# Kernel tuning notes

Measured on AMD Instinct MI355X. Metric: run time of the kernel, lower is better.

## Reference

```python
import jax, jax.numpy as jnp
import numpy as np
from jax import lax

EPS = 1e-5


def setup_inputs() -> dict:
    key = jax.random.key(0)
    ks = jax.random.split(key, 8)
    b, c_in, h, w = 16, 256, 64, 64
    c_out, kh, n_exp = 512, 3, 8
    fan_in = c_in * kh * kh
    bound_w = float(np.sqrt(6.0 / fan_in))  # kaiming_uniform a=sqrt(5) -> U(-sqrt(6/fan_in), +)
    bound_b = float(1.0 / np.sqrt(fan_in))
    return {
        "x": jax.random.normal(ks[0], (b, c_in, h, w), dtype=jnp.float32),
        "expert_weight": jax.random.uniform(ks[1], (n_exp, c_out, c_in, kh, kh), jnp.float32, -bound_w, bound_w),
        "expert_bias": jax.random.uniform(ks[2], (n_exp, c_out), jnp.float32, -bound_b, bound_b),
        "fc_w": jax.random.uniform(ks[3], (n_exp, c_in), jnp.float32, -1.0 / np.sqrt(c_in), 1.0 / np.sqrt(c_in)),
        "fc_b": jax.random.uniform(ks[4], (n_exp,), jnp.float32, -1.0 / np.sqrt(c_in), 1.0 / np.sqrt(c_in)),
        "bn_gamma": jnp.ones((c_out,), jnp.float32),
        "bn_beta": jnp.zeros((c_out,), jnp.float32),
    }


def reference(x, expert_weight, expert_bias, fc_w, fc_b, bn_gamma, bn_beta):
    # --- route_func: GAP -> Linear -> sigmoid -> (b, k) ---
    pooled = x.mean(axis=(2, 3))                       # (b, c_in)
    routing = jax.nn.sigmoid(pooled @ fc_w.T + fc_b)   # (b, k)

    # --- per-sample combined kernels and biases ---
    comb_w = jnp.einsum('bk,koihw->boihw', routing, expert_weight)  # (b, c_out, c_in, kh, kw)
    comb_b = routing @ expert_bias                                  # (b, c_out)

    # --- per-sample conv (equivalent of groups=b grouped conv) ---
    def conv_one(xi, wi):
        # xi: (c_in, h, w), wi: (c_out, c_in, kh, kw)
        return lax.conv_general_dilated(
            xi[None], wi, window_strides=(1, 1), padding=[(1, 1), (1, 1)],
            rhs_dilation=(1, 1), dimension_numbers=('NCHW', 'OIHW', 'NCHW'))[0]

    out = jax.vmap(conv_one)(x, comb_w) + comb_b[:, :, None, None]  # (b, c_out, h, w)

    # --- BatchNorm2d (training mode: batch statistics) ---
    mean = out.mean(axis=(0, 2, 3))
    var = out.var(axis=(0, 2, 3))
    out = (out - mean[None, :, None, None]) * (bn_gamma * lax.rsqrt(var + EPS))[None, :, None, None] \
          + bn_beta[None, :, None, None]

    # --- LeakyReLU(0.1) ---
    return jnp.where(out > 0, out, 0.1 * out)
```

## Files before the change

### kernel.cpp

```cpp
#include <hip/hip_runtime.h>
#include <hip/hip_bf16.h>
#include <stdint.h>

typedef unsigned short u16;
typedef short bf16x8 __attribute__((ext_vector_type(8)));
typedef float f32x4 __attribute__((ext_vector_type(4)));
typedef u16 u16x8 __attribute__((ext_vector_type(8)));

#define DEVFN static __device__ __forceinline__

#define NB 16
#define CIN 256
#define HH 64
#define WW 64
#define COUT 512
#define NPX 4096
#define NSTEP 72

DEVFN u16 bf16_rne(float f){
  union { float f; uint32_t u; } v; v.f = f;
  uint32_t u = v.u;
  return (u16)((u + 0x7fffu + ((u >> 16) & 1u)) >> 16);
}

DEVFN void gload16(const void* g, void* l){
  __builtin_amdgcn_global_load_lds((const __attribute__((address_space(1))) void*)g,
                                   (__attribute__((address_space(3))) void*)l,
                                   16, 0, 0);
}

#define VMWAIT(N) asm volatile("s_waitcnt vmcnt(" #N ")" ::: "memory")
#define BARRIER() do { __builtin_amdgcn_s_barrier(); \
                       __builtin_amdgcn_sched_barrier(0); \
                       asm volatile("" ::: "memory"); } while(0)

__global__ void k_route(const float* __restrict__ pooled, const float* __restrict__ fcw,
                        const float* __restrict__ fcb, float* __restrict__ routing){
  int bk = blockIdx.x;
  int b = bk >> 3, k = bk & 7;
  int l = threadIdx.x;
  float4 pv = ((const float4*)(pooled + b*CIN))[l];
  float4 wv = ((const float4*)(fcw   + k*CIN))[l];
  float s = pv.x*wv.x + pv.y*wv.y + pv.z*wv.z + pv.w*wv.w;
  for (int o = 32; o; o >>= 1) s += __shfl_down(s, o);
  if (l == 0) routing[b*8 + k] = 1.0f / (1.0f + __expf(-(s * (1.0f/(float)NPX) + fcb[k])));
}

__global__ void k_cbias(const float* __restrict__ routing, const float* __restrict__ eb,
                        float* __restrict__ cbias){
  int idx = blockIdx.x*256 + threadIdx.x;
  int b = idx >> 9, co = idx & 511;
  float s = 0.f;
  for (int k = 0; k < 8; k++) s += routing[b*8+k] * eb[k*COUT + co];
  cbias[idx] = s;
}

__global__ void k_wcomb(const float* __restrict__ routing, const float* __restrict__ ew,
                        u16* __restrict__ wc){
  int blk  = blockIdx.x;
  int step = blk >> 6;
  int cog  = blk & 63;
  int cb = step / 9, rs = step - cb*9;
  int t = threadIdx.x;
  int ci = t & 31, co = cog*8 + (t >> 5);
  int cig = cb*32 + ci;
  float wv[8];
#pragma unroll
  for (int k = 0; k < 8; k++)
    wv[k] = ew[(size_t)((k*COUT + co)*CIN + cig)*9 + rs];
  for (int b = 0; b < NB; b++){
    float s = 0.f;
#pragma unroll
    for (int k = 0; k < 8; k++) s += routing[b*8+k] * wv[k];
    wc[((size_t)(b*NSTEP + step)*COUT + co)*32 + ci] = bf16_rne(s);
  }
}

__global__ void k_halo(u16* __restrict__ xt){
  int blk = blockIdx.x;
  int b = blk / 66, row = blk - b*66;
  uint32_t* base = (uint32_t*)(xt + ((size_t)(b*66 + row))*68*256);
  int t = threadIdx.x;
  if (row == 0 || row == 65){
    for (int i = t; i < 8704; i += 256) base[i] = 0;
  } else {
    for (int i = t; i < 512; i += 256){
      int idx = (i < 128) ? i : (8320 + (i - 128));
      base[idx] = 0;
    }
  }
}

__global__ void k_xprep(const float* __restrict__ x, u16* __restrict__ xt,
                        float* __restrict__ pooled){
  int blk = blockIdx.x;
  int ctile = blk & 3;
  int h = (blk >> 2) & 63;
  int b = blk >> 8;
  __shared__ u16 S[64][66];
  int t = threadIdx.x;
  {
    int ci_l = t >> 2, w0 = (t & 3) * 16;
    const float4* src = (const float4*)(x + ((size_t)((b*CIN + ctile*64 + ci_l)*HH + h)*WW + w0));
    float4 a = src[0], bb = src[1], c = src[2], d = src[3];
    u16* row = &S[ci_l][w0];
    row[0]=bf16_rne(a.x);  row[1]=bf16_rne(a.y);  row[2]=bf16_rne(a.z);  row[3]=bf16_rne(a.w);
    row[4]=bf16_rne(bb.x); row[5]=bf16_rne(bb.y); row[6]=bf16_rne(bb.z); row[7]=bf16_rne(bb.w);
    row[8]=bf16_rne(c.x);  row[9]=bf16_rne(c.y);  row[10]=bf16_rne(c.z); row[11]=bf16_rne(c.w);
    row[12]=bf16_rne(d.x); row[13]=bf16_rne(d.y); row[14]=bf16_rne(d.z); row[15]=bf16_rne(d.w);
    float s = a.x+a.y+a.z+a.w + bb.x+bb.y+bb.z+bb.w + c.x+c.y+c.z+c.w + d.x+d.y+d.z+d.w;
    s += __shfl_down(s, 2);
    s += __shfl_down(s, 1);
    if ((t & 3) == 0) atomicAdd(&pooled[b*CIN + ctile*64 + ci_l], s);
  }
  __syncthreads();
  {
    int w_l = t >> 2, cig = (t & 3) * 16;
    u16x8 v0, v1;
#pragma unroll
    for (int j = 0; j < 8; j++){ v0[j] = S[cig+j][w_l]; v1[j] = S[cig+8+j][w_l]; }
    u16* dst = xt + ((size_t)(b*66 + h + 1)*68 + (w_l + 1))*CIN + ctile*64 + cig;
    *(u16x8*)(dst)     = v0;
    *(u16x8*)(dst + 8) = v1;
  }
}

#define XBYTES 17408
#define WBYTES 8192

DEVFN void stage_w(const u16* __restrict__ wstep, char* dst, int wv, int l){
#pragma unroll
  for (int i = 0; i < 2; i++){
    int q = i*256 + wv*64 + l;
    int co_l = q >> 2, j = q & 3;
    gload16(wstep + co_l*32 + ((j ^ ((co_l >> 1) & 3)) << 3), dst + (i*256 + wv*64)*16);
  }
  __builtin_amdgcn_sched_barrier(0);
}

DEVFN void stage_x(const u16* __restrict__ xtb, int h0, int cioff, char* dst, int wv, int l){
#pragma unroll
  for (int i = 0; i < 5; i++){
    int qb = i*256 + wv*64;
    if (qb >= 1088) qb -= 1088;
    int q = qb + l;
    int t2 = q >> 2;
    int lr = (t2 * 964) >> 16;
    int c  = t2 - lr*68;
    int j  = q & 3;
    gload16(xtb + ((size_t)(h0 + lr)*68 + c)*CIN + cioff + ((j ^ ((c >> 1) & 3)) << 3),
            dst + qb*16);
  }
  __builtin_amdgcn_sched_barrier(0);
}

template<int RS>
DEVFN void conv_step(int cb, char* ldsbase, char* Xb,
                     const u16* __restrict__ wcb,
                     int wv, int l, int wn, int l15, int kbq, int byteA0,
                     f32x4 acc[4][4])
{
  constexpr int r = RS / 3, s = RS - r*3;
  const char* Wc = ldsbase + (RS % 3)*WBYTES;
  char* Wp       = ldsbase + ((RS + 2) % 3)*WBYTES;

  int c0 = l15 + s;
  int byteB0 = ((wn + r)*68 + c0)*64 + ((kbq ^ ((c0 >> 1) & 3)) << 4);
  bf16x8 af[4], bfr[4];
#pragma unroll
  for (int m = 0; m < 4; m++) af[m]  = *(const bf16x8*)(Wc + byteA0 + m*1024);
#pragma unroll
  for (int n = 0; n < 4; n++) bfr[n] = *(const bf16x8*)(Xb + byteB0 + n*1024);

  if constexpr (RS <= 6) {
    stage_w(wcb + (size_t)(cb*9 + RS + 2)*(COUT*32), Wp, wv, l);
  } else {
    if (cb != 7) stage_w(wcb + (size_t)(cb*9 + RS + 2)*(COUT*32), Wp, wv, l);
  }

  if constexpr (RS == 7) {
    if (cb == 7) { VMWAIT(0); } else { VMWAIT(2); }
  } else {
    VMWAIT(2);
  }
  BARRIER();

  __builtin_amdgcn_s_setprio(1);
#pragma unroll
  for (int m = 0; m < 4; m++)
#pragma unroll
    for (int n = 0; n < 4; n++)
      acc[m][n] = __builtin_amdgcn_mfma_f32_16x16x32_bf16(af[m], bfr[n], acc[m][n], 0, 0, 0);
  __builtin_amdgcn_s_setprio(0);
}

DEVFN void conv_step8(int cb, char* ldsbase, char* Xb,
                      const u16* __restrict__ xtb, const u16* __restrict__ wcb, int h0,
                      int wv, int l, int wn, int l15, int kbq, int byteA0,
                      f32x4 acc[4][4])
{
  const char* Wc = ldsbase + 2*WBYTES;
  char* Wp       = ldsbase + 1*WBYTES;
  int c0 = l15 + 2;
  int byteB0 = ((wn + 2)*68 + c0)*64 + ((kbq ^ ((c0 >> 1) & 3)) << 4);
  bf16x8 af[4], bfr[4];
#pragma unroll
  for (int m = 0; m < 4; m++) af[m]  = *(const bf16x8*)(Wc + byteA0 + m*1024);
#pragma unroll
  for (int n = 0; n < 4; n++) bfr[n] = *(const bf16x8*)(Xb + byteB0 + n*1024);

  BARRIER();

  stage_w(wcb + (size_t)(cb*9 + 10)*(COUT*32), Wp, wv, l);
  stage_x(xtb, h0, (cb+1)*32, Xb, wv, l);

  __builtin_amdgcn_s_setprio(1);
#pragma unroll
  for (int m = 0; m < 4; m++)
#pragma unroll
    for (int n = 0; n < 4; n++)
      acc[m][n] = __builtin_amdgcn_mfma_f32_16x16x32_bf16(af[m], bfr[n], acc[m][n], 0, 0, 0);
  __builtin_amdgcn_s_setprio(0);

  VMWAIT(0);
  BARRIER();
}

DEVFN void conv_step8_last(char* ldsbase, char* Xb,
                           int wn, int l15, int kbq, int byteA0,
                           f32x4 acc[4][4])
{
  const char* Wc = ldsbase + 2*WBYTES;
  int c0 = l15 + 2;
  int byteB0 = ((wn + 2)*68 + c0)*64 + ((kbq ^ ((c0 >> 1) & 3)) << 4);
  bf16x8 af[4], bfr[4];
#pragma unroll
  for (int m = 0; m < 4; m++) af[m]  = *(const bf16x8*)(Wc + byteA0 + m*1024);
#pragma unroll
  for (int n = 0; n < 4; n++) bfr[n] = *(const bf16x8*)(Xb + byteB0 + n*1024);
#pragma unroll
  for (int m = 0; m < 4; m++)
#pragma unroll
    for (int n = 0; n < 4; n++)
      acc[m][n] = __builtin_amdgcn_mfma_f32_16x16x32_bf16(af[m], bfr[n], acc[m][n], 0, 0, 0);
}

__global__ __launch_bounds__(256, 3) void k_conv(
    const u16* __restrict__ xt, const u16* __restrict__ wc,
    const float* __restrict__ cbias, float* __restrict__ out, u16* __restrict__ obf,
    float* __restrict__ ssum, float* __restrict__ ssq)
{
  __shared__ char lds[3*WBYTES + XBYTES];
  char* Xb = lds + 3*WBYTES;

  int hw = blockIdx.x;
  int lb = (hw & 7) * 256 + (hw >> 3);
  int b  = lb >> 7;
  int ct = (lb >> 5) & 3;
  int pt = lb & 31;
  int h0 = pt * 2;

  int t = threadIdx.x, l = t & 63, wv = t >> 6;
  int wm = wv >> 1, wn = wv & 1;
  int l15 = l & 15, kbq = l >> 4;

  const u16* xtb = xt + (size_t)b * 66*68*CIN;
  const u16* wcb = wc + (size_t)(b*NSTEP) * COUT*32 + ct*128*32;

  f32x4 acc[4][4];
#pragma unroll
  for (int m = 0; m < 4; m++)
#pragma unroll
    for (int n = 0; n < 4; n++) acc[m][n] = (f32x4){0.f,0.f,0.f,0.f};

  const int byteA0 = (wm*64 + l15)*64 + ((kbq ^ ((l15 >> 1) & 3)) << 4);

  stage_x(xtb, h0, 0, Xb, wv, l);
  stage_w(wcb,           lds + 0*WBYTES, wv, l);
  stage_w(wcb + COUT*32, lds + 1*WBYTES, wv, l);
  VMWAIT(2);
  BARRIER();

  for (int cb = 0; cb < 8; cb++){
    conv_step<0>(cb, lds, Xb, wcb, wv,l,wn,l15,kbq,byteA0, acc);
    conv_step<1>(cb, lds, Xb, wcb, wv,l,wn,l15,kbq,byteA0, acc);
    conv_step<2>(cb, lds, Xb, wcb, wv,l,wn,l15,kbq,byteA0, acc);
    conv_step<3>(cb, lds, Xb, wcb, wv,l,wn,l15,kbq,byteA0, acc);
    conv_step<4>(cb, lds, Xb, wcb, wv,l,wn,l15,kbq,byteA0, acc);
    conv_step<5>(cb, lds, Xb, wcb, wv,l,wn,l15,kbq,byteA0, acc);
    conv_step<6>(cb, lds, Xb, wcb, wv,l,wn,l15,kbq,byteA0, acc);
    conv_step<7>(cb, lds, Xb, wcb, wv,l,wn,l15,kbq,byteA0, acc);
    if (cb < 7) conv_step8(cb, lds, Xb, xtb, wcb, h0, wv,l,wn,l15,kbq,byteA0, acc);
    else        conv_step8_last(lds, Xb, wn,l15,kbq,byteA0, acc);
  }

  int co_t = ct*128 + wm*64 + (kbq << 2);
  int px_t = pt*128 + wn*64 + l15;
#pragma unroll
  for (int m = 0; m < 4; m++){
#pragma unroll
    for (int rg = 0; rg < 4; rg++){
      int co = co_t + m*16 + rg;
      float bias = cbias[b*COUT + co];
      float s1 = 0.f, s2 = 0.f;
      size_t base = ((size_t)b * COUT + co) * NPX + px_t;
#pragma unroll
      for (int n = 0; n < 4; n++){
        float v = acc[m][n][rg] + bias;
        if (obf) obf[base + n*16] = bf16_rne(v);
        else     out[base + n*16] = v;
        s1 += v; s2 += v*v;
      }
#pragma unroll
      for (int o = 8; o; o >>= 1){ s1 += __shfl_xor(s1, o); s2 += __shfl_xor(s2, o); }
      if (l15 == 0){ atomicAdd(&ssum[co], s1); atomicAdd(&ssq[co], s2); }
    }
  }
}

__global__ void k_stats(const float* __restrict__ ssum, const float* __restrict__ ssq,
                        const float* __restrict__ gamma, const float* __restrict__ beta,
                        float* __restrict__ sc, float* __restrict__ sh){
  int co = blockIdx.x*256 + threadIdx.x;
  const float invN = 1.0f / 65536.0f;
  float m  = ssum[co] * invN;
  float var = ssq[co] * invN - m*m;
  float scale = gamma[co] * rsqrtf(var + 1e-5f);
  sc[co] = scale;
  sh[co] = beta[co] - m*scale;
}

__global__ void k_norm(float* __restrict__ out, const float* __restrict__ sc,
                       const float* __restrict__ sh){
  const int NF4 = (NB*COUT*NPX)/4;
  int idx = blockIdx.x*256 + threadIdx.x;
  float4* o4 = (float4*)out;
  for (int i = idx; i < NF4; i += 2048*256){
    float4 v = o4[i];
    int co = (i >> 10) & 511;
    float a = sc[co], d = sh[co];
    v.x = fmaf(v.x, a, d); v.y = fmaf(v.y, a, d);
    v.z = fmaf(v.z, a, d); v.w = fmaf(v.w, a, d);
    v.x = v.x > 0.f ? v.x : 0.1f*v.x;
    v.y = v.y > 0.f ? v.y : 0.1f*v.y;
    v.z = v.z > 0.f ? v.z : 0.1f*v.z;
    v.w = v.w > 0.f ? v.w : 0.1f*v.w;
    o4[i] = v;
  }
}

__global__ void k_norm_bf16(const u16* __restrict__ obf, float* __restrict__ out,
                            const float* __restrict__ sc, const float* __restrict__ sh){
  const int NG = (NB*COUT*NPX)/8;
  int idx = blockIdx.x*256 + threadIdx.x;
  for (int g = idx; g < NG; g += 2048*256){
    u16x8 v = *(const u16x8*)(obf + (size_t)g*8);
    int co = (g >> 9) & 511;
    float a = sc[co], d = sh[co];
    float vv[8];
#pragma unroll
    for (int j = 0; j < 8; j++){
      union{ uint32_t u; float f; } c; c.u = ((uint32_t)(u16)v[j]) << 16;
      float w = fmaf(c.f, a, d);
      vv[j] = w > 0.f ? w : 0.1f*w;
    }
    float4* o4 = (float4*)(out + (size_t)g*8);
    o4[0] = (float4){vv[0],vv[1],vv[2],vv[3]};
    o4[1] = (float4){vv[4],vv[5],vv[6],vv[7]};
  }
}

extern "C" void kernel_launch(void* const* d_in, const int* in_sizes, int n_in,
                              void* d_out, int out_size, void* d_ws, size_t ws_size,
                              hipStream_t stream) {
  const float* x     = (const float*)d_in[0];
  const float* ew    = (const float*)d_in[1];
  const float* eb    = (const float*)d_in[2];
  const float* fcw   = (const float*)d_in[3];
  const float* fcb   = (const float*)d_in[4];
  const float* gamma = (const float*)d_in[5];
  const float* beta  = (const float*)d_in[6];
  float* out = (float*)d_out;

  char* ws = (char*)d_ws;
  const size_t XT_BYTES  = (size_t)NB*66*68*CIN*2;
  const size_t WC_BYTES  = (size_t)NB*NSTEP*COUT*32*2;
  const size_t FL_BYTES  = 65536;
  const size_t OBF_BYTES = (size_t)NB*COUT*NPX*2;
  u16* xt = (u16*)ws;
  u16* wc = (u16*)(ws + XT_BYTES);
  float* fbase   = (float*)(ws + XT_BYTES + WC_BYTES);
  float* pooled  = fbase;
  float* ssum    = fbase + 4096;
  float* ssq     = fbase + 4608;
  float* routing = fbase + 5120;
  float* cbias   = fbase + 5248;
  float* sc      = fbase + 13440;
  float* sh      = fbase + 13952;
  bool use_bf16 = ws_size >= XT_BYTES + WC_BYTES + FL_BYTES + OBF_BYTES;
  u16* obf = use_bf16 ? (u16*)(ws + XT_BYTES + WC_BYTES + FL_BYTES) : (u16*)nullptr;

  hipMemsetAsync(pooled, 0, 5120*sizeof(float), stream);

  k_halo <<<1056, 256, 0, stream>>>(xt);
  k_xprep<<<4096, 256, 0, stream>>>(x, xt, pooled);
  k_route<<<128,   64, 0, stream>>>(pooled, fcw, fcb, routing);
  k_cbias<<<32,   256, 0, stream>>>(routing, eb, cbias);
  k_wcomb<<<4608, 256, 0, stream>>>(routing, ew, wc);
  k_conv <<<2048, 256, 0, stream>>>(xt, wc, cbias, out, obf, ssum, ssq);
  k_stats<<<2,    256, 0, stream>>>(ssum, ssq, gamma, beta, sc, sh);
  if (use_bf16) k_norm_bf16<<<2048, 256, 0, stream>>>(obf, out, sc, sh);
  else          k_norm     <<<2048, 256, 0, stream>>>(out, sc, sh);
}
```

Measured before the change: 311.6 us.

## Process conv taps in pairs with four-buffer weight ring to halve barriers

Restructures the conv main loop to consume two 3x3 taps per barrier interval, using four LDS weight buffers that rotate in pairs instead of a three-buffer ring with one barrier per tap. Each pair loads A/B fragments for both taps, issues two weight prefetches, runs 32 MFMAs, then waits for all loads and syncs once. This cuts barrier and wait overhead, at the cost of one more weight buffer of LDS (which may lower occupancy from the 3 blocks per CU in the launch bounds), more registers for the doubled fragments, and a full vmcnt(0) wait per pair.

After: 317.8 us. Within noise of the previous version (+2.0%).

```diff
diff --git a/kernel.cpp b/kernel.cpp
--- a/kernel.cpp
+++ b/kernel.cpp
@@ -154,65 +154,73 @@
   __builtin_amdgcn_sched_barrier(0);
 }
 
-template<int RS>
-DEVFN void conv_step(int cb, char* ldsbase, char* Xb,
+template<int RS0>
+DEVFN void conv_pair(int cb, const char* Wa, const char* Wb, char* Wc, char* Wd,
+                     const char* Xb,
                      const u16* __restrict__ wcb,
                      int wv, int l, int wn, int l15, int kbq, int byteA0,
                      f32x4 acc[4][4])
 {
-  constexpr int r = RS / 3, s = RS - r*3;
-  const char* Wc = ldsbase + (RS % 3)*WBYTES;
-  char* Wp       = ldsbase + ((RS + 2) % 3)*WBYTES;
-
-  int c0 = l15 + s;
-  int byteB0 = ((wn + r)*68 + c0)*64 + ((kbq ^ ((c0 >> 1) & 3)) << 4);
-  bf16x8 af[4], bfr[4];
-#pragma unroll
-  for (int m = 0; m < 4; m++) af[m]  = *(const bf16x8*)(Wc + byteA0 + m*1024);
-#pragma unroll
-  for (int n = 0; n < 4; n++) bfr[n] = *(const bf16x8*)(Xb + byteB0 + n*1024);
-
-  if constexpr (RS <= 6) {
-    stage_w(wcb + (size_t)(cb*9 + RS + 2)*(COUT*32), Wp, wv, l);
-  } else {
-    if (cb != 7) stage_w(wcb + (size_t)(cb*9 + RS + 2)*(COUT*32), Wp, wv, l);
-  }
-
-  if constexpr (RS == 7) {
-    if (cb == 7) { VMWAIT(0); } else { VMWAIT(2); }
-  } else {
-    VMWAIT(2);
-  }
+  constexpr int r0 = RS0/3,     s0 = RS0 - r0*3;
+  constexpr int r1 = (RS0+1)/3, s1 = (RS0+1) - r1*3;
+
+  bf16x8 a0[4], a1[4], b0[4], b1[4];
+#pragma unroll
+  for (int m = 0; m < 4; m++){
+    a0[m] = *(const bf16x8*)(Wa + byteA0 + m*1024);
+    a1[m] = *(const bf16x8*)(Wb + byteA0 + m*1024);
+  }
+  {
+    int c0 = l15 + s0;
+    int bb = ((wn + r0)*68 + c0)*64 + ((kbq ^ ((c0 >> 1) & 3)) << 4);
+#pragma unroll
+    for (int n = 0; n < 4; n++) b0[n] = *(const bf16x8*)(Xb + bb + n*1024);
+  }
+  {
+    int c1 = l15 + s1;
+    int bb = ((wn + r1)*68 + c1)*64 + ((kbq ^ ((c1 >> 1) & 3)) << 4);
+#pragma unroll
+    for (int n = 0; n < 4; n++) b1[n] = *(const bf16x8*)(Xb + bb + n*1024);
+  }
+
+  stage_w(wcb + (size_t)(cb*9 + RS0 + 2)*(COUT*32), Wc, wv, l);
+  if (RS0 != 6 || cb != 7)
+    stage_w(wcb + (size_t)(cb*9 + RS0 + 3)*(COUT*32), Wd, wv, l);
+
+  __builtin_amdgcn_s_setprio(1);
+#pragma unroll
+  for (int m = 0; m < 4; m++)
+#pragma unroll
+    for (int n = 0; n < 4; n++)
+      acc[m][n] = __builtin_amdgcn_mfma_f32_16x16x32_bf16(a0[m], b0[n], acc[m][n], 0, 0, 0);
+#pragma unroll
+  for (int m = 0; m < 4; m++)
+#pragma unroll
+    for (int n = 0; n < 4; n++)
+      acc[m][n] = __builtin_amdgcn_mfma_f32_16x16x32_bf16(a1[m], b1[n], acc[m][n], 0, 0, 0);
+  __builtin_amdgcn_s_setprio(0);
+
+  VMWAIT(0);
   BARRIER();
-
-  __builtin_amdgcn_s_setprio(1);
-#pragma unroll
-  for (int m = 0; m < 4; m++)
-#pragma unroll
-    for (int n = 0; n < 4; n++)
-      acc[m][n] = __builtin_amdgcn_mfma_f32_16x16x32_bf16(af[m], bfr[n], acc[m][n], 0, 0, 0);
-  __builtin_amdgcn_s_setprio(0);
-}
-
-DEVFN void conv_step8(int cb, char* ldsbase, char* Xb,
+}
+
+DEVFN void conv_bound(int cb, const char* Wa, char* Wc, char* Xb,
                       const u16* __restrict__ xtb, const u16* __restrict__ wcb, int h0,
                       int wv, int l, int wn, int l15, int kbq, int byteA0,
                       f32x4 acc[4][4])
 {
-  const char* Wc = ldsbase + 2*WBYTES;
-  char* Wp       = ldsbase + 1*WBYTES;
   int c0 = l15 + 2;
-  int byteB0 = ((wn + 2)*68 + c0)*64 + ((kbq ^ ((c0 >> 1) & 3)) << 4);
+  int bb = ((wn + 2)*68 + c0)*64 + ((kbq ^ ((c0 >> 1) & 3)) << 4);
   bf16x8 af[4], bfr[4];
 #pragma unroll
-  for (int m = 0; m < 4; m++) af[m]  = *(const bf16x8*)(Wc + byteA0 + m*1024);
-#pragma unroll
-  for (int n = 0; n < 4; n++) bfr[n] = *(const bf16x8*)(Xb + byteB0 + n*1024);
+  for (int m = 0; m < 4; m++) af[m]  = *(const bf16x8*)(Wa + byteA0 + m*1024);
+#pragma unroll
+  for (int n = 0; n < 4; n++) bfr[n] = *(const bf16x8*)(Xb + bb + n*1024);
 
   BARRIER();
 
-  stage_w(wcb + (size_t)(cb*9 + 10)*(COUT*32), Wp, wv, l);
   stage_x(xtb, h0, (cb+1)*32, Xb, wv, l);
+  stage_w(wcb + (size_t)(cb*9 + 10)*(COUT*32), Wc, wv, l);
 
   __builtin_amdgcn_s_setprio(1);
 #pragma unroll
@@ -226,18 +234,17 @@
   BARRIER();
 }
 
-DEVFN void conv_step8_last(char* ldsbase, char* Xb,
+DEVFN void conv_bound_last(const char* Wa, const char* Xb,
                            int wn, int l15, int kbq, int byteA0,
                            f32x4 acc[4][4])
 {
-  const char* Wc = ldsbase + 2*WBYTES;
   int c0 = l15 + 2;
-  int byteB0 = ((wn + 2)*68 + c0)*64 + ((kbq ^ ((c0 >> 1) & 3)) << 4);
+  int bb = ((wn + 2)*68 + c0)*64 + ((kbq ^ ((c0 >> 1) & 3)) << 4);
   bf16x8 af[4], bfr[4];
 #pragma unroll
-  for (int m = 0; m < 4; m++) af[m]  = *(const bf16x8*)(Wc + byteA0 + m*1024);
-#pragma unroll
-  for (int n = 0; n < 4; n++) bfr[n] = *(const bf16x8*)(Xb + byteB0 + n*1024);
+  for (int m = 0; m < 4; m++) af[m]  = *(const bf16x8*)(Wa + byteA0 + m*1024);
+#pragma unroll
+  for (int n = 0; n < 4; n++) bfr[n] = *(const bf16x8*)(Xb + bb + n*1024);
 #pragma unroll
   for (int m = 0; m < 4; m++)
 #pragma unroll
@@ -250,8 +257,8 @@
     const float* __restrict__ cbias, float* __restrict__ out, u16* __restrict__ obf,
     float* __restrict__ ssum, float* __restrict__ ssq)
 {
-  __shared__ char lds[3*WBYTES + XBYTES];
-  char* Xb = lds + 3*WBYTES;
+  __shared__ char lds[4*WBYTES + XBYTES];
+  char* Xb = lds + 4*WBYTES;
 
   int hw = blockIdx.x;
   int lb = (hw & 7) * 256 + (hw >> 3);
@@ -278,20 +285,29 @@
   stage_x(xtb, h0, 0, Xb, wv, l);
   stage_w(wcb,           lds + 0*WBYTES, wv, l);
   stage_w(wcb + COUT*32, lds + 1*WBYTES, wv, l);
-  VMWAIT(2);
+  VMWAIT(0);
   BARRIER();
 
+  char* Wa = lds + 0*WBYTES;
+  char* Wb = lds + 1*WBYTES;
+  char* Wc = lds + 2*WBYTES;
+  char* Wd = lds + 3*WBYTES;
+
   for (int cb = 0; cb < 8; cb++){
-    conv_step<0>(cb, lds, Xb, wcb, wv,l,wn,l15,kbq,byteA0, acc);
-    conv_step<1>(cb, lds, Xb, wcb, wv,l,wn,l15,kbq,byteA0, acc);
-    conv_step<2>(cb, lds, Xb, wcb, wv,l,wn,l15,kbq,byteA0, acc);
-    conv_step<3>(cb, lds, Xb, wcb, wv,l,wn,l15,kbq,byteA0, acc);
-    conv_step<4>(cb, lds, Xb, wcb, wv,l,wn,l15,kbq,byteA0, acc);
-    conv_step<5>(cb, lds, Xb, wcb, wv,l,wn,l15,kbq,byteA0, acc);
-    conv_step<6>(cb, lds, Xb, wcb, wv,l,wn,l15,kbq,byteA0, acc);
-    conv_step<7>(cb, lds, Xb, wcb, wv,l,wn,l15,kbq,byteA0, acc);
-    if (cb < 7) conv_step8(cb, lds, Xb, xtb, wcb, h0, wv,l,wn,l15,kbq,byteA0, acc);
-    else        conv_step8_last(lds, Xb, wn,l15,kbq,byteA0, acc);
+    conv_pair<0>(cb, Wa,Wb,Wc,Wd, Xb, wcb, wv,l,wn,l15,kbq,byteA0, acc);
+    { char* t0=Wa; char* t1=Wb; Wa=Wc; Wb=Wd; Wc=t0; Wd=t1; }
+    conv_pair<2>(cb, Wa,Wb,Wc,Wd, Xb, wcb, wv,l,wn,l15,kbq,byteA0, acc);
+    { char* t0=Wa; char* t1=Wb; Wa=Wc; Wb=Wd; Wc=t0; Wd=t1; }
+    conv_pair<4>(cb, Wa,Wb,Wc,Wd, Xb, wcb, wv,l,wn,l15,kbq,byteA0, acc);
+    { char* t0=Wa; char* t1=Wb; Wa=Wc; Wb=Wd; Wc=t0; Wd=t1; }
+    conv_pair<6>(cb, Wa,Wb,Wc,Wd, Xb, wcb, wv,l,wn,l15,kbq,byteA0, acc);
+    { char* t0=Wa; char* t1=Wb; Wa=Wc; Wb=Wd; Wc=t0; Wd=t1; }
+    if (cb < 7){
+      conv_bound(cb, Wa, Wc, Xb, xtb, wcb, h0, wv,l,wn,l15,kbq,byteA0, acc);
+      { char* t0=Wa; Wa=Wb; Wb=Wc; Wc=t0; }
+    } else {
+      conv_bound_last(Wa, Xb, wn,l15,kbq,byteA0, acc);
+    }
   }
 
   int co_t = ct*128 + wm*64 + (kbq << 2);
```

## Use 2-wave conv blocks with 64x128 warp tiles and double-buffered weights

Applied to the files above, without the earlier changes.

The conv kernel drops from 4 waves to 2 waves per block. Each wave now computes 64 output channels by 128 pixels (a 4x8 MFMA accumulator grid), which raises register-level reuse of A and B fragments. Weight staging changes from a 3-deep ring with a lookahead of two steps to a 2-buffer ping-pong with a full vmcnt(0) wait and a barrier after every step. Per-lane swizzle offsets are precomputed. The trade-off is twice the accumulator registers, less latency hiding within each block, and occupancy set to launch_bounds(128,2).

Result: slower. 501.3 us (+60.9%).

```diff
diff --git a/kernel.cpp b/kernel.cpp
--- a/kernel.cpp
+++ b/kernel.cpp
@@ -30,6 +30,8 @@
 }
 
 #define VMWAIT(N) asm volatile("s_waitcnt vmcnt(" #N ")" ::: "memory")
+#define LGKMWAIT0() do { asm volatile("s_waitcnt lgkmcnt(0)" ::: "memory"); \
+                         __builtin_amdgcn_sched_barrier(0); } while(0)
 #define BARRIER() do { __builtin_amdgcn_s_barrier(); \
                        __builtin_amdgcn_sched_barrier(0); \
                        asm volatile("" ::: "memory"); } while(0)
@@ -130,18 +132,19 @@
 
 DEVFN void stage_w(const u16* __restrict__ wstep, char* dst, int wv, int l){
 #pragma unroll
-  for (int i = 0; i < 2; i++){
-    int q = i*256 + wv*64 + l;
+  for (int i = 0; i < 4; i++){
+    int qb = i*128 + wv*64;
+    int q  = qb + l;
     int co_l = q >> 2, j = q & 3;
-    gload16(wstep + co_l*32 + ((j ^ ((co_l >> 1) & 3)) << 3), dst + (i*256 + wv*64)*16);
+    gload16(wstep + co_l*32 + ((j ^ ((co_l >> 1) & 3)) << 3), dst + qb*16);
   }
   __builtin_amdgcn_sched_barrier(0);
 }
 
 DEVFN void stage_x(const u16* __restrict__ xtb, int h0, int cioff, char* dst, int wv, int l){
 #pragma unroll
-  for (int i = 0; i < 5; i++){
-    int qb = i*256 + wv*64;
+  for (int i = 0; i < 9; i++){
+    int qb = i*128 + wv*64;
     if (qb >= 1088) qb -= 1088;
     int q = qb + l;
     int t2 = q >> 2;
@@ -155,70 +158,61 @@
 }
 
 template<int RS>
-DEVFN void conv_step(int cb, char* ldsbase, char* Xb,
+DEVFN void conv_step(int cb, const char* Wc, char* Wn, const char* Xb,
                      const u16* __restrict__ wcb,
-                     int wv, int l, int wn, int l15, int kbq, int byteA0,
-                     f32x4 acc[4][4])
+                     int wv, int l, int byteA0, const int pre[3],
+                     f32x4 acc[4][8])
 {
   constexpr int r = RS / 3, s = RS - r*3;
-  const char* Wc = ldsbase + (RS % 3)*WBYTES;
-  char* Wp       = ldsbase + ((RS + 2) % 3)*WBYTES;
-
-  int c0 = l15 + s;
-  int byteB0 = ((wn + r)*68 + c0)*64 + ((kbq ^ ((c0 >> 1) & 3)) << 4);
-  bf16x8 af[4], bfr[4];
-#pragma unroll
-  for (int m = 0; m < 4; m++) af[m]  = *(const bf16x8*)(Wc + byteA0 + m*1024);
-#pragma unroll
-  for (int n = 0; n < 4; n++) bfr[n] = *(const bf16x8*)(Xb + byteB0 + n*1024);
-
-  if constexpr (RS <= 6) {
-    stage_w(wcb + (size_t)(cb*9 + RS + 2)*(COUT*32), Wp, wv, l);
-  } else {
-    if (cb != 7) stage_w(wcb + (size_t)(cb*9 + RS + 2)*(COUT*32), Wp, wv, l);
-  }
-
-  if constexpr (RS == 7) {
-    if (cb == 7) { VMWAIT(0); } else { VMWAIT(2); }
-  } else {
-    VMWAIT(2);
-  }
-  BARRIER();
+
+  bf16x8 af[4], bfr[8];
+#pragma unroll
+  for (int m = 0; m < 4; m++) af[m] = *(const bf16x8*)(Wc + byteA0 + m*1024);
+#pragma unroll
+  for (int n = 0; n < 8; n++){
+    const int byteB = ((n >> 2) + r)*4352 + (n & 3)*1024;
+    bfr[n] = *(const bf16x8*)(Xb + byteB + pre[s]);
+  }
+
+  stage_w(wcb + (size_t)(cb*9 + RS + 1)*(COUT*32), Wn, wv, l);
 
   __builtin_amdgcn_s_setprio(1);
 #pragma unroll
   for (int m = 0; m < 4; m++)
 #pragma unroll
-    for (int n = 0; n < 4; n++)
+    for (int n = 0; n < 8; n++)
       acc[m][n] = __builtin_amdgcn_mfma_f32_16x16x32_bf16(af[m], bfr[n], acc[m][n], 0, 0, 0);
   __builtin_amdgcn_s_setprio(0);
-}
-
-DEVFN void conv_step8(int cb, char* ldsbase, char* Xb,
+
+  VMWAIT(0);
+  BARRIER();
+}
+
+DEVFN void conv_bound(int cb, const char* Wc, char* Wn, char* Xb,
                       const u16* __restrict__ xtb, const u16* __restrict__ wcb, int h0,
-                      int wv, int l, int wn, int l15, int kbq, int byteA0,
-                      f32x4 acc[4][4])
+                      int wv, int l, int byteA0, const int pre[3],
+                      f32x4 acc[4][8])
 {
-  const char* Wc = ldsbase + 2*WBYTES;
-  char* Wp       = ldsbase + 1*WBYTES;
-  int c0 = l15 + 2;
-  int byteB0 = ((wn + 2)*68 + c0)*64 + ((kbq ^ ((c0 >> 1) & 3)) << 4);
-  bf16x8 af[4], bfr[4];
-#pragma unroll
-  for (int m = 0; m < 4; m++) af[m]  = *(const bf16x8*)(Wc + byteA0 + m*1024);
-#pragma unroll
-  for (int n = 0; n < 4; n++) bfr[n] = *(const bf16x8*)(Xb + byteB0 + n*1024);
-
+  bf16x8 af[4], bfr[8];
+#pragma unroll
+  for (int m = 0; m < 4; m++) af[m] = *(const bf16x8*)(Wc + byteA0 + m*1024);
+#pragma unroll
+  for (int n = 0; n < 8; n++){
+    const int byteB = ((n >> 2) + 2)*4352 + (n & 3)*1024;
+    bfr[n] = *(const bf16x8*)(Xb + byteB + pre[2]);
+  }
+
+  LGKMWAIT0();
   BARRIER();
 
-  stage_w(wcb + (size_t)(cb*9 + 10)*(COUT*32), Wp, wv, l);
   stage_x(xtb, h0, (cb+1)*32, Xb, wv, l);
+  stage_w(wcb + (size_t)((cb+1)*9)*(COUT*32), Wn, wv, l);
 
   __builtin_amdgcn_s_setprio(1);
 #pragma unroll
   for (int m = 0; m < 4; m++)
 #pragma unroll
-    for (int n = 0; n < 4; n++)
+    for (int n = 0; n < 8; n++)
       acc[m][n] = __builtin_amdgcn_mfma_f32_16x16x32_bf16(af[m], bfr[n], acc[m][n], 0, 0, 0);
   __builtin_amdgcn_s_setprio(0);
 
@@ -226,32 +220,31 @@
   BARRIER();
 }
 
-DEVFN void conv_step8_last(char* ldsbase, char* Xb,
-                           int wn, int l15, int kbq, int byteA0,
-                           f32x4 acc[4][4])
+DEVFN void conv_last(const char* Wc, const char* Xb,
+                     int byteA0, const int pre[3], f32x4 acc[4][8])
 {
-  const char* Wc = ldsbase + 2*WBYTES;
-  int c0 = l15 + 2;
-  int byteB0 = ((wn + 2)*68 + c0)*64 + ((kbq ^ ((c0 >> 1) & 3)) << 4);
-  bf16x8 af[4], bfr[4];
-#pragma unroll
-  for (int m = 0; m < 4; m++) af[m]  = *(const bf16x8*)(Wc + byteA0 + m*1024);
-#pragma unroll
-  for (int n = 0; n < 4; n++) bfr[n] = *(const bf16x8*)(Xb + byteB0 + n*1024);
+  bf16x8 af[4], bfr[8];
+#pragma unroll
+  for (int m = 0; m < 4; m++) af[m] = *(const bf16x8*)(Wc + byteA0 + m*1024);
+#pragma unroll
+  for (int n = 0; n < 8; n++){
+    const int byteB = ((n >> 2) + 2)*4352 + (n & 3)*1024;
+    bfr[n] = *(const bf16x8*)(Xb + byteB + pre[2]);
+  }
 #pragma unroll
   for (int m = 0; m < 4; m++)
 #pragma unroll
-    for (int n = 0; n < 4; n++)
+    for (int n = 0; n < 8; n++)
       acc[m][n] = __builtin_amdgcn_mfma_f32_16x16x32_bf16(af[m], bfr[n], acc[m][n], 0, 0, 0);
 }
 
-__global__ __launch_bounds__(256, 3) void k_conv(
+__global__ __launch_bounds__(128, 2) void k_conv(
     const u16* __restrict__ xt, const u16* __restrict__ wc,
     const float* __restrict__ cbias, float* __restrict__ out, u16* __restrict__ obf,
     float* __restrict__ ssum, float* __restrict__ ssq)
 {
-  __shared__ char lds[3*WBYTES + XBYTES];
-  char* Xb = lds + 3*WBYTES;
+  __shared__ char lds[2*WBYTES + XBYTES];
+  char* Xb = lds + 2*WBYTES;
 
   int hw = blockIdx.x;
   int lb = (hw & 7) * 256 + (hw >> 3);
@@ -261,41 +254,51 @@
   int h0 = pt * 2;
 
   int t = threadIdx.x, l = t & 63, wv = t >> 6;
-  int wm = wv >> 1, wn = wv & 1;
   int l15 = l & 15, kbq = l >> 4;
 
   const u16* xtb = xt + (size_t)b * 66*68*CIN;
   const u16* wcb = wc + (size_t)(b*NSTEP) * COUT*32 + ct*128*32;
 
-  f32x4 acc[4][4];
+  f32x4 acc[4][8];
 #pragma unroll
   for (int m = 0; m < 4; m++)
 #pragma unroll
-    for (int n = 0; n < 4; n++) acc[m][n] = (f32x4){0.f,0.f,0.f,0.f};
-
-  const int byteA0 = (wm*64 + l15)*64 + ((kbq ^ ((l15 >> 1) & 3)) << 4);
+    for (int n = 0; n < 8; n++) acc[m][n] = (f32x4){0.f,0.f,0.f,0.f};
+
+  const int byteA0 = (wv*64 + l15)*64 + ((kbq ^ ((l15 >> 1) & 3)) << 4);
+  int pre[3];
+#pragma unroll
+  for (int s = 0; s < 3; s++){
+    int c0 = l15 + s;
+    pre[s] = c0*64 + ((kbq ^ ((c0 >> 1) & 3)) << 4);
+  }
 
   stage_x(xtb, h0, 0, Xb, wv, l);
-  stage_w(wcb,           lds + 0*WBYTES, wv, l);
-  stage_w(wcb + COUT*32, lds + 1*WBYTES, wv, l);
-  VMWAIT(2);
+  stage_w(wcb, lds, wv, l);
+  VMWAIT(0);
   BARRIER();
 
+  char* Wc = lds;
+  char* Wn = lds + WBYTES;
   for (int cb = 0; cb < 8; cb++){
-    conv_step<0>(cb, lds, Xb, wcb, wv,l,wn,l15,kbq,byteA0, acc);
-    conv_step<1>(cb, lds, Xb, wcb, wv,l,wn,l15,kbq,byteA0, acc);
-    conv_step<2>(cb, lds, Xb, wcb, wv,l,wn,l15,kbq,byteA0, acc);
-    conv_step<3>(cb, lds, Xb, wcb, wv,l,wn,l15,kbq,byteA0, acc);
-    conv_step<4>(cb, lds, Xb, wcb, wv,l,wn,l15,kbq,byteA0, acc);
-    conv_step<5>(cb, lds, Xb, wcb, wv,l,wn,l15,kbq,byteA0, acc);
-    conv_step<6>(cb, lds, Xb, wcb, wv,l,wn,l15,kbq,byteA0, acc);
-    conv_step<7>(cb, lds, Xb, wcb, wv,l,wn,l15,kbq,byteA0, acc);
-    if (cb < 7) conv_step8(cb, lds, Xb, xtb, wcb, h0, wv,l,wn,l15,kbq,byteA0, acc);
-    else        conv_step8_last(lds, Xb, wn,l15,kbq,byteA0, acc);
-  }
-
-  int co_t = ct*128 + wm*64 + (kbq << 2);
-  int px_t = pt*128 + wn*64 + l15;
+    conv_step<0>(cb, Wc, Wn, Xb, wcb, wv,l,byteA0,pre, acc); { char* tp=Wc; Wc=Wn; Wn=tp; }
+    conv_step<1>(cb, Wc, Wn, Xb, wcb, wv,l,byteA0,pre, acc); { char* tp=Wc; Wc=Wn; Wn=tp; }
+    conv_step<2>(cb, Wc, Wn, Xb, wcb, wv,l,byteA0,pre, acc); { char* tp=Wc; Wc=Wn; Wn=tp; }
+    conv_step<3>(cb, Wc, Wn, Xb, wcb, wv,l,byteA0,pre, acc); { char* tp=Wc; Wc=Wn; Wn=tp; }
+    conv_step<4>(cb, Wc, Wn, Xb, wcb, wv,l,byteA0,pre, acc); { char* tp=Wc; Wc=Wn; Wn=tp; }
+    conv_step<5>(cb, Wc, Wn, Xb, wcb, wv,l,byteA0,pre, acc); { char* tp=Wc; Wc=Wn; Wn=tp; }
+    conv_step<6>(cb, Wc, Wn, Xb, wcb, wv,l,byteA0,pre, acc); { char* tp=Wc; Wc=Wn; Wn=tp; }
+    conv_step<7>(cb, Wc, Wn, Xb, wcb, wv,l,byteA0,pre, acc); { char* tp=Wc; Wc=Wn; Wn=tp; }
+    if (cb < 7){
+      conv_bound(cb, Wc, Wn, Xb, xtb, wcb, h0, wv,l,byteA0,pre, acc);
+      { char* tp=Wc; Wc=Wn; Wn=tp; }
+    } else {
+      conv_last(Wc, Xb, byteA0, pre, acc);
+    }
+  }
+
+  int co_t = ct*128 + wv*64 + (kbq << 2);
+  float* outb = out;
 #pragma unroll
   for (int m = 0; m < 4; m++){
 #pragma unroll
@@ -303,12 +306,13 @@
       int co = co_t + m*16 + rg;
       float bias = cbias[b*COUT + co];
       float s1 = 0.f, s2 = 0.f;
-      size_t base = ((size_t)b * COUT + co) * NPX + px_t;
-#pragma unroll
-      for (int n = 0; n < 4; n++){
+      size_t base = ((size_t)b * COUT + co) * NPX;
+#pragma unroll
+      for (int n = 0; n < 8; n++){
         float v = acc[m][n][rg] + bias;
-        if (obf) obf[base + n*16] = bf16_rne(v);
-        else     out[base + n*16] = v;
+        int px = pt*128 + (n >> 2)*64 + (n & 3)*16 + l15;
+        if (obf) obf[base + px] = bf16_rne(v);
+        else     outb[base + px] = v;
         s1 += v; s2 += v*v;
       }
 #pragma unroll
@@ -407,7 +411,7 @@
   k_route<<<128,   64, 0, stream>>>(pooled, fcw, fcb, routing);
   k_cbias<<<32,   256, 0, stream>>>(routing, eb, cbias);
   k_wcomb<<<4608, 256, 0, stream>>>(routing, ew, wc);
-  k_conv <<<2048, 256, 0, stream>>>(xt, wc, cbias, out, obf, ssum, ssq);
+  k_conv <<<2048, 128, 0, stream>>>(xt, wc, cbias, out, obf, ssum, ssq);
   k_stats<<<2,    256, 0, stream>>>(ssum, ssq, gamma, beta, sc, sh);
   if (use_bf16) k_norm_bf16<<<2048, 256, 0, stream>>>(obf, out, sc, sh);
   else          k_norm     <<<2048, 256, 0, stream>>>(out, sc, sh);
```

## Read conv input fragments directly from global memory instead of LDS staging

Applied to the files above, without the earlier changes.

Removes the LDS staging buffer for the transposed input tile and has each lane load its B-operand fragments straight from global memory (via L1/L2) for every filter tap. Weights still go through the triple-buffered LDS ring, and the separate step-8 stage/barrier variants fold into the templated step. The smaller LDS footprint lets launch bounds rise to 4 blocks per CU. The cost is nine times more global or L1 traffic for input with load latency exposed right before the MFMAs, since those loads are no longer prefetched a stage ahead. VMWAIT counts were not adjusted for the extra direct loads.

Result: slower. 509.9 us (+63.6%).

```diff
diff --git a/kernel.cpp b/kernel.cpp
--- a/kernel.cpp
+++ b/kernel.cpp
@@ -125,7 +125,6 @@
   }
 }
 
-#define XBYTES 17408
 #define WBYTES 8192
 
 DEVFN void stage_w(const u16* __restrict__ wstep, char* dst, int wv, int l){
@@ -138,39 +137,23 @@
   __builtin_amdgcn_sched_barrier(0);
 }
 
-DEVFN void stage_x(const u16* __restrict__ xtb, int h0, int cioff, char* dst, int wv, int l){
-#pragma unroll
-  for (int i = 0; i < 5; i++){
-    int qb = i*256 + wv*64;
-    if (qb >= 1088) qb -= 1088;
-    int q = qb + l;
-    int t2 = q >> 2;
-    int lr = (t2 * 964) >> 16;
-    int c  = t2 - lr*68;
-    int j  = q & 3;
-    gload16(xtb + ((size_t)(h0 + lr)*68 + c)*CIN + cioff + ((j ^ ((c >> 1) & 3)) << 3),
-            dst + qb*16);
-  }
-  __builtin_amdgcn_sched_barrier(0);
-}
-
 template<int RS>
-DEVFN void conv_step(int cb, char* ldsbase, char* Xb,
+DEVFN void conv_step(int cb, char* ldsbase, const u16* __restrict__ xrow,
                      const u16* __restrict__ wcb,
-                     int wv, int l, int wn, int l15, int kbq, int byteA0,
-                     f32x4 acc[4][4])
+                     int wv, int l, int byteA0, f32x4 acc[4][4])
 {
   constexpr int r = RS / 3, s = RS - r*3;
   const char* Wc = ldsbase + (RS % 3)*WBYTES;
   char* Wp       = ldsbase + ((RS + 2) % 3)*WBYTES;
 
-  int c0 = l15 + s;
-  int byteB0 = ((wn + r)*68 + c0)*64 + ((kbq ^ ((c0 >> 1) & 3)) << 4);
-  bf16x8 af[4], bfr[4];
-#pragma unroll
-  for (int m = 0; m < 4; m++) af[m]  = *(const bf16x8*)(Wc + byteA0 + m*1024);
-#pragma unroll
-  for (int n = 0; n < 4; n++) bfr[n] = *(const bf16x8*)(Xb + byteB0 + n*1024);
+  bf16x8 af[4];
+#pragma unroll
+  for (int m = 0; m < 4; m++) af[m] = *(const bf16x8*)(Wc + byteA0 + m*1024);
+
+  const u16* bp = xrow + (r*68 + s)*CIN + cb*32;
+  bf16x8 bfr[4];
+#pragma unroll
+  for (int n = 0; n < 4; n++) bfr[n] = *(const bf16x8*)(bp + n*16*CIN);
 
   if constexpr (RS <= 6) {
     stage_w(wcb + (size_t)(cb*9 + RS + 2)*(COUT*32), Wp, wv, l);
@@ -178,13 +161,6 @@
     if (cb != 7) stage_w(wcb + (size_t)(cb*9 + RS + 2)*(COUT*32), Wp, wv, l);
   }
 
-  if constexpr (RS == 7) {
-    if (cb == 7) { VMWAIT(0); } else { VMWAIT(2); }
-  } else {
-    VMWAIT(2);
-  }
-  BARRIER();
-
   __builtin_amdgcn_s_setprio(1);
 #pragma unroll
   for (int m = 0; m < 4; m++)
@@ -192,66 +168,24 @@
     for (int n = 0; n < 4; n++)
       acc[m][n] = __builtin_amdgcn_mfma_f32_16x16x32_bf16(af[m], bfr[n], acc[m][n], 0, 0, 0);
   __builtin_amdgcn_s_setprio(0);
-}
-
-DEVFN void conv_step8(int cb, char* ldsbase, char* Xb,
-                      const u16* __restrict__ xtb, const u16* __restrict__ wcb, int h0,
-                      int wv, int l, int wn, int l15, int kbq, int byteA0,
-                      f32x4 acc[4][4])
-{
-  const char* Wc = ldsbase + 2*WBYTES;
-  char* Wp       = ldsbase + 1*WBYTES;
-  int c0 = l15 + 2;
-  int byteB0 = ((wn + 2)*68 + c0)*64 + ((kbq ^ ((c0 >> 1) & 3)) << 4);
-  bf16x8 af[4], bfr[4];
-#pragma unroll
-  for (int m = 0; m < 4; m++) af[m]  = *(const bf16x8*)(Wc + byteA0 + m*1024);
-#pragma unroll
-  for (int n = 0; n < 4; n++) bfr[n] = *(const bf16x8*)(Xb + byteB0 + n*1024);
-
-  BARRIER();
-
-  stage_w(wcb + (size_t)(cb*9 + 10)*(COUT*32), Wp, wv, l);
-  stage_x(xtb, h0, (cb+1)*32, Xb, wv, l);
-
-  __builtin_amdgcn_s_setprio(1);
-#pragma unroll
-  for (int m = 0; m < 4; m++)
-#pragma unroll
-    for (int n = 0; n < 4; n++)
-      acc[m][n] = __builtin_amdgcn_mfma_f32_16x16x32_bf16(af[m], bfr[n], acc[m][n], 0, 0, 0);
-  __builtin_amdgcn_s_setprio(0);
-
-  VMWAIT(0);
-  BARRIER();
-}
-
-DEVFN void conv_step8_last(char* ldsbase, char* Xb,
-                           int wn, int l15, int kbq, int byteA0,
-                           f32x4 acc[4][4])
-{
-  const char* Wc = ldsbase + 2*WBYTES;
-  int c0 = l15 + 2;
-  int byteB0 = ((wn + 2)*68 + c0)*64 + ((kbq ^ ((c0 >> 1) & 3)) << 4);
-  bf16x8 af[4], bfr[4];
-#pragma unroll
-  for (int m = 0; m < 4; m++) af[m]  = *(const bf16x8*)(Wc + byteA0 + m*1024);
-#pragma unroll
-  for (int n = 0; n < 4; n++) bfr[n] = *(const bf16x8*)(Xb + byteB0 + n*1024);
-#pragma unroll
-  for (int m = 0; m < 4; m++)
-#pragma unroll
-    for (int n = 0; n < 4; n++)
-      acc[m][n] = __builtin_amdgcn_mfma_f32_16x16x32_bf16(af[m], bfr[n], acc[m][n], 0, 0, 0);
-}
-
-__global__ __launch_bounds__(256, 3) void k_conv(
+
+  if constexpr (RS == 8) {
+    if (cb == 7) return;
+    VMWAIT(2); BARRIER();
+  } else if constexpr (RS == 7) {
+    if (cb == 7) { VMWAIT(0); } else { VMWAIT(2); }
+    BARRIER();
+  } else {
+    VMWAIT(2); BARRIER();
+  }
+}
+
+__global__ __launch_bounds__(256, 4) void k_conv(
     const u16* __restrict__ xt, const u16* __restrict__ wc,
     const float* __restrict__ cbias, float* __restrict__ out, u16* __restrict__ obf,
     float* __restrict__ ssum, float* __restrict__ ssq)
 {
-  __shared__ char lds[3*WBYTES + XBYTES];
-  char* Xb = lds + 3*WBYTES;
+  __shared__ char lds[3*WBYTES];
 
   int hw = blockIdx.x;
   int lb = (hw & 7) * 256 + (hw >> 3);
@@ -264,8 +198,9 @@
   int wm = wv >> 1, wn = wv & 1;
   int l15 = l & 15, kbq = l >> 4;
 
-  const u16* xtb = xt + (size_t)b * 66*68*CIN;
   const u16* wcb = wc + (size_t)(b*NSTEP) * COUT*32 + ct*128*32;
+  const u16* xrow = xt + (size_t)b * 66*68*CIN
+                       + ((size_t)(h0 + wn)*68 + l15)*CIN + kbq*8;
 
   f32x4 acc[4][4];
 #pragma unroll
@@ -275,23 +210,21 @@
 
   const int byteA0 = (wm*64 + l15)*64 + ((kbq ^ ((l15 >> 1) & 3)) << 4);
 
-  stage_x(xtb, h0, 0, Xb, wv, l);
   stage_w(wcb,           lds + 0*WBYTES, wv, l);
   stage_w(wcb + COUT*32, lds + 1*WBYTES, wv, l);
   VMWAIT(2);
   BARRIER();
 
   for (int cb = 0; cb < 8; cb++){
-    conv_step<0>(cb, lds, Xb, wcb, wv,l,wn,l15,kbq,byteA0, acc);
-    conv_step<1>(cb, lds, Xb, wcb, wv,l,wn,l15,kbq,byteA0, acc);
-    conv_step<2>(cb, lds, Xb, wcb, wv,l,wn,l15,kbq,byteA0, acc);
-    conv_step<3>(cb, lds, Xb, wcb, wv,l,wn,l15,kbq,byteA0, acc);
-    conv_step<4>(cb, lds, Xb, wcb, wv,l,wn,l15,kbq,byteA0, acc);
-    conv_step<5>(cb, lds, Xb, wcb, wv,l,wn,l15,kbq,byteA0, acc);
-    conv_step<6>(cb, lds, Xb, wcb, wv,l,wn,l15,kbq,byteA0, acc);
-    conv_step<7>(cb, lds, Xb, wcb, wv,l,wn,l15,kbq,byteA0, acc);
-    if (cb < 7) conv_step8(cb, lds, Xb, xtb, wcb, h0, wv,l,wn,l15,kbq,byteA0, acc);
-    else        conv_step8_last(lds, Xb, wn,l15,kbq,byteA0, acc);
+    conv_step<0>(cb, lds, xrow, wcb, wv,l,byteA0, acc);
+    conv_step<1>(cb, lds, xrow, wcb, wv,l,byteA0, acc);
+    conv_step<2>(cb, lds, xrow, wcb, wv,l,byteA0, acc);
+    conv_step<3>(cb, lds, xrow, wcb, wv,l,byteA0, acc);
+    conv_step<4>(cb, lds, xrow, wcb, wv,l,byteA0, acc);
+    conv_step<5>(cb, lds, xrow, wcb, wv,l,byteA0, acc);
+    conv_step<6>(cb, lds, xrow, wcb, wv,l,byteA0, acc);
+    conv_step<7>(cb, lds, xrow, wcb, wv,l,byteA0, acc);
+    conv_step<8>(cb, lds, xrow, wcb, wv,l,byteA0, acc);
   }
 
   int co_t = ct*128 + wm*64 + (kbq << 2);
```
